# Kernel tuning notes

Hardware: AMD Instinct MI355X
Metric: run time of the kernel (lower is better)

## Reference

```python
import jax, jax.numpy as jnp
import numpy as np

D_MODEL = 512; N_LAYERS = 12; D_STATE = 64; D_CONV = 4; EXPAND = 2
HEADDIM = 64; KLEN = 10
D_INNER = EXPAND * D_MODEL              # 1024
NHEADS = D_INNER // HEADDIM             # 16
CONV_DIM = D_INNER + 2 * D_STATE        # 1152
D_IN_PROJ = 2 * D_INNER + 2 * D_STATE + NHEADS  # 2192
CHUNK = 128; EPS = 1e-5
B_SZ = 2; SEQ = 2048


def rmsnorm(x, w):
    return x * jax.lax.rsqrt(jnp.mean(x * x, axis=-1, keepdims=True) + EPS) * w


def nerf_pe(x):
    # NeRF positional encoding of raw 3D coords, zero-padded to D_MODEL
    nf = D_MODEL // (2 * x.shape[-1])  # 85 freqs per coord -> 510 dims
    freqs = 2.0 ** jnp.arange(nf, dtype=x.dtype)
    ang = x[..., None] * freqs                       # [B,L,3,nf]
    pe = jnp.concatenate([jnp.sin(ang), jnp.cos(ang)], axis=-1)
    pe = pe.reshape(*x.shape[:-1], -1)               # [B,L,510]
    return jnp.pad(pe, ((0, 0), (0, 0), (0, D_MODEL - pe.shape[-1])))


def ssd(xh, dt, A, Bm, Cm):
    # Chunked Mamba2 SSD selective scan.
    # xh [B,L,H,P], dt [B,L,H] (post-softplus), A [H] (negative), Bm/Cm [B,L,N]
    Bb, L, H, P = xh.shape; N = Bm.shape[-1]; C = L // CHUNK
    xh = xh.reshape(Bb, C, CHUNK, H, P)
    dt = dt.reshape(Bb, C, CHUNK, H)
    Bm = Bm.reshape(Bb, C, CHUNK, N)
    Cm = Cm.reshape(Bb, C, CHUNK, N)
    a = dt * A                                   # [B,C,Q,H], <= 0
    a_cum = jnp.cumsum(a, axis=2)
    # intra-chunk decay L[i,j] = exp(a_cum_i - a_cum_j), i >= j
    diff = a_cum[:, :, :, None, :] - a_cum[:, :, None, :, :]  # [B,C,i,j,H]
    tri = jnp.tril(jnp.ones((CHUNK, CHUNK), bool))
    Lmat = jnp.where(tri[None, None, :, :, None], jnp.exp(diff), 0.0)
    scores = jnp.einsum('bcin,bcjn->bcij', Cm, Bm)
    M = scores[..., None] * Lmat * dt[:, :, None, :, :]       # [B,C,i,j,H]
    y_diag = jnp.einsum('bcijh,bcjhp->bcihp', M, xh)
    # per-chunk end states
    a_sum = a_cum[:, :, -1, :]                                # [B,C,H]
    dstate = jnp.exp(a_sum[:, :, None, :] - a_cum) * dt       # [B,C,Q,H]
    S = jnp.einsum('bcjh,bcjn,bcjhp->bchpn', dstate, Bm, xh)  # [B,C,H,P,N]
    dec = jnp.exp(a_sum)

    def step(h, inp):
        Sc, dc = inp
        return h * dc[:, :, None, None] + Sc, h  # emit state BEFORE this chunk

    h0 = jnp.zeros((Bb, H, P, N), xh.dtype)
    _, hs = jax.lax.scan(step, h0, (S.transpose(1, 0, 2, 3, 4), dec.transpose(1, 0, 2)))
    y_off = jnp.einsum('bcih,bcin,cbhpn->bcihp', jnp.exp(a_cum), Cm, hs)
    return (y_diag + y_off).reshape(Bb, L, H, P)


def mamba_block(x, in_w, conv_w, conv_b, dt_b, A_log, Dp, gw, out_w):
    Bb, L, _ = x.shape
    zxbcdt = x @ in_w                             # [B,L,2192]
    z = zxbcdt[..., :D_INNER]
    xBC = zxbcdt[..., D_INNER:D_INNER + CONV_DIM]
    dt = zxbcdt[..., D_INNER + CONV_DIM:]
    # causal depthwise conv1d, kernel D_CONV
    xp = jnp.pad(xBC, ((0, 0), (D_CONV - 1, 0), (0, 0)))
    xc = sum(xp[:, k:k + L, :] * conv_w[:, k] for k in range(D_CONV)) + conv_b
    xc = jax.nn.silu(xc)
    xh = xc[..., :D_INNER].reshape(Bb, L, NHEADS, HEADDIM)
    Bm = xc[..., D_INNER:D_INNER + D_STATE]
    Cm = xc[..., D_INNER + D_STATE:]
    dt = jax.nn.softplus(dt + dt_b)
    A = -jnp.exp(A_log)
    y = ssd(xh, dt, A, Bm, Cm) + Dp[None, None, :, None] * xh
    y = y.reshape(Bb, L, D_INNER)
    y = rmsnorm(y * jax.nn.silu(z), gw)           # gated RMSNorm
    return y @ out_w


def setup_inputs() -> dict:
    key = jax.random.key(0)
    ks = jax.random.split(key, 8)
    s = 0.02
    x = jax.random.normal(ks[0], (B_SZ, SEQ, 3), jnp.float32)
    W_embed = jax.random.normal(ks[1], (3, D_MODEL), jnp.float32) * s
    rms_w = jnp.ones((N_LAYERS, D_MODEL), jnp.float32)
    in_proj_w = jax.random.normal(ks[2], (N_LAYERS, D_MODEL, D_IN_PROJ), jnp.float32) * s
    conv_w = jax.random.normal(ks[3], (N_LAYERS, CONV_DIM, D_CONV), jnp.float32) * s
    conv_b = jnp.zeros((N_LAYERS, CONV_DIM), jnp.float32)
    dt_bias = jax.random.normal(ks[4], (N_LAYERS, NHEADS), jnp.float32) * 0.1
    A_log = jnp.log(jnp.broadcast_to(jnp.arange(1, NHEADS + 1, dtype=jnp.float32), (N_LAYERS, NHEADS)))
    D_param = jnp.ones((N_LAYERS, NHEADS), jnp.float32)
    gnorm_w = jnp.ones((N_LAYERS, D_INNER), jnp.float32)
    out_proj_w = jax.random.normal(ks[5], (N_LAYERS, D_INNER, D_MODEL), jnp.float32) * s
    final_norm_w = jnp.ones((D_MODEL,), jnp.float32)
    head_w = jax.random.normal(ks[6], (D_MODEL, KLEN * 3), jnp.float32) * s
    head_b = jnp.zeros((KLEN * 3,), jnp.float32)
    return dict(x=x, W_embed=W_embed, rms_w=rms_w, in_proj_w=in_proj_w,
                conv_w=conv_w, conv_b=conv_b, dt_bias=dt_bias, A_log=A_log,
                D_param=D_param, gnorm_w=gnorm_w, out_proj_w=out_proj_w,
                final_norm_w=final_norm_w, head_w=head_w, head_b=head_b)


def reference(x, W_embed, rms_w, in_proj_w, conv_w, conv_b, dt_bias, A_log,
              D_param, gnorm_w, out_proj_w, final_norm_w, head_w, head_b):
    x = jnp.where(x == -100.0, 0.0, x)            # change_maskval
    h = x @ W_embed + nerf_pe(x)                  # EmbedderAdd

    def layer(h, p):
        rw, iw, cw, cb, db, al, dp, gw, ow = p
        z = mamba_block(rmsnorm(h, rw), iw, cw, cb, db, al, dp, gw, ow)
        return h + z, None                        # dropout is identity in eval

    h, _ = jax.lax.scan(layer, h, (rms_w, in_proj_w, conv_w, conv_b, dt_bias,
                                   A_log, D_param, gnorm_w, out_proj_w))
    h = rmsnorm(h, final_norm_w)
    return h @ head_w + head_b                    # [B,L,30]
```

## Files before the change

### kernel.cpp

```cpp
#include <hip/hip_runtime.h>
#include <math.h>

#define DM 512
#define DSTATE 64
#define HD 64
#define DI 1024
#define NH 16
#define CONVD 1152
#define DIP 2192
#define CHK 128
#define NCH 16
#define BSZ 2
#define SEQL 2048
#define BL (BSZ*SEQL)
#define NLAYER 12
#define EPSF 1e-5f
#define NPAD_IN 2304

typedef __attribute__((ext_vector_type(4))) float f32x4;
typedef __attribute__((ext_vector_type(8))) short s16x8;

__device__ __forceinline__ float bf2f(ushort u) {
    union { unsigned int i; float f; } v; v.i = ((unsigned int)u) << 16; return v.f;
}
__device__ __forceinline__ ushort f2bf(float f) {
    union { float f; unsigned int u; } v; v.f = f;
    unsigned int u = v.u;
    unsigned int r = (u + 0x7fffu + ((u >> 16) & 1u)) >> 16;
    return (ushort)r;
}

#define GLOAD_LDS16(gptr, lptr) __builtin_amdgcn_global_load_lds( \
    (const __attribute__((address_space(1))) void*)(gptr), \
    (__attribute__((address_space(3))) void*)(lptr), 16, 0, 0)

#define MFMA_BF16(a, b, c) __builtin_amdgcn_mfma_f32_16x16x32_bf16(a, b, c, 0, 0, 0)

__global__ void embed_kernel(const float* __restrict__ x, const float* __restrict__ W,
                             float* __restrict__ h) {
    int tok = blockIdx.x;
    float xe[3];
#pragma unroll
    for (int e = 0; e < 3; e++) {
        float v = x[tok * 3 + e];
        xe[e] = (v == -100.0f) ? 0.0f : v;
    }
    for (int d = threadIdx.x; d < DM; d += blockDim.x) {
        float pe = 0.0f;
        if (d < 510) {
            int e = d / 170, r = d % 170;
            int is_sin = (r < 85);
            int k = is_sin ? r : r - 85;
            float ang = xe[e] * ldexpf(1.0f, k);
            double dv = is_sin ? sin((double)ang) : cos((double)ang);
            pe = (float)dv;
        }
        float acc = pe;
#pragma unroll
        for (int e = 0; e < 3; e++) acc += xe[e] * W[e * DM + d];
        h[(size_t)tok * DM + d] = acc;
    }
}

__global__ __launch_bounds__(256) void rmsnorm512_bf_kernel(const float* __restrict__ in,
                                                            const float* __restrict__ w,
                                                            ushort* __restrict__ out) {
    int tok = blockIdx.x;
    const float* row = in + (size_t)tok * DM;
    float v0 = row[threadIdx.x];
    float v1 = row[threadIdx.x + 256];
    float ss = v0 * v0 + v1 * v1;
    for (int o = 32; o; o >>= 1) ss += __shfl_down(ss, o);
    __shared__ float sbuf[4];
    if ((threadIdx.x & 63) == 0) sbuf[threadIdx.x >> 6] = ss;
    __syncthreads();
    if (threadIdx.x == 0) {
        float s = sbuf[0] + sbuf[1] + sbuf[2] + sbuf[3];
        sbuf[0] = rsqrtf(s / (float)DM + EPSF);
    }
    __syncthreads();
    float rs = sbuf[0];
    ushort* orow = out + (size_t)tok * DM;
    orow[threadIdx.x] = f2bf(v0 * rs * w[threadIdx.x]);
    orow[threadIdx.x + 256] = f2bf(v1 * rs * w[threadIdx.x + 256]);
}

__global__ __launch_bounds__(256) void gatenorm_kernel(const float* __restrict__ y,
                                                       const ushort* __restrict__ zx,
                                                       const float* __restrict__ gw,
                                                       ushort* __restrict__ yb) {
    int tok = blockIdx.x;
    const ushort* zrow = zx + (size_t)tok * DIP;
    const float* yrow = y + (size_t)tok * DI;
    float v[4];
    float ss = 0.0f;
#pragma unroll
    for (int k = 0; k < 4; k++) {
        int d = threadIdx.x + k * 256;
        float z = bf2f(zrow[d]);
        float s = z / (1.0f + __expf(-z));
        float val = yrow[d] * s;
        v[k] = val;
        ss += val * val;
    }
    for (int o = 32; o; o >>= 1) ss += __shfl_down(ss, o);
    __shared__ float sbuf[4];
    if ((threadIdx.x & 63) == 0) sbuf[threadIdx.x >> 6] = ss;
    __syncthreads();
    if (threadIdx.x == 0) {
        float s = sbuf[0] + sbuf[1] + sbuf[2] + sbuf[3];
        sbuf[0] = rsqrtf(s / (float)DI + EPSF);
    }
    __syncthreads();
    float rs = sbuf[0];
    ushort* ob = yb + (size_t)tok * DI;
#pragma unroll
    for (int k = 0; k < 4; k++) {
        int d = threadIdx.x + k * 256;
        ob[d] = f2bf(v[k] * rs * gw[d]);
    }
}

__global__ __launch_bounds__(256) void convT_kernel(const float* __restrict__ w,
                                                    ushort* __restrict__ wT,
                                                    int K, int N, int Npad) {
    __shared__ ushort tile[64][65];
    int l = blockIdx.z;
    int n0 = blockIdx.x * 64, k0 = blockIdx.y * 64;
    const float* src = w + (size_t)l * K * N;
    ushort* dst = wT + (size_t)l * Npad * K;
    int tid = threadIdx.x;
#pragma unroll
    for (int t = 0; t < 16; t++) {
        int idx = tid + t * 256;
        int r = idx >> 6, c = idx & 63;
        float v = (n0 + c < N) ? src[(size_t)(k0 + r) * N + n0 + c] : 0.0f;
        tile[c][r] = f2bf(v);
    }
    __syncthreads();
#pragma unroll
    for (int t = 0; t < 16; t++) {
        int idx = tid + t * 256;
        int r = idx >> 6, c = idx & 63;
        dst[(size_t)(n0 + r) * K + k0 + c] = tile[r][c];
    }
}

template <int MODE, int MT>
__global__ __launch_bounds__(256) void gemm_bf16_kernel(
    const ushort* __restrict__ A, const ushort* __restrict__ BT,
    ushort* __restrict__ Cb, float* __restrict__ Cf, float* __restrict__ aux,
    int N, int Nstride, int K)
{
    __shared__ ushort As[2][MT * 32 * 64];
    __shared__ ushort Bs[2][128 * 64];
    int nwg = gridDim.x * gridDim.y;
    int w0 = blockIdx.y * gridDim.x + blockIdx.x;
    int wg = (w0 & 7) * (nwg >> 3) + (w0 >> 3);
    int by = wg / gridDim.x, bx = wg - by * gridDim.x;
    int bm = by * (MT * 32), bn = bx * 128;
    int tid = threadIdx.x;
    int lane = tid & 63, wid = tid >> 6;
    int wr = wid >> 1, wc = wid & 1;
    int r15 = lane & 15, q = lane >> 4;
    f32x4 acc[MT][4] = {};
    const int nkt = K >> 6;

#define STAGE_GEMM(b, kt) do {                                              \
        int k0s = (kt) << 6;                                                \
        _Pragma("unroll")                                                   \
        for (int t = 0; t < MT; t++) {                                      \
            int cbase = wid * (MT * 64) + t * 64;                           \
            int chunk = cbase + lane;                                       \
            int row = chunk >> 3, s = chunk & 7;                            \
            int kc = s ^ (row & 7);                                         \
            GLOAD_LDS16(A + (size_t)(bm + row) * K + k0s + kc * 8,          \
                        &As[b][cbase * 8]);                                 \
        }                                                                   \
        _Pragma("unroll")                                                   \
        for (int t = 0; t < 4; t++) {                                       \
            int cbase = wid * 256 + t * 64;                                 \
            int chunk = cbase + lane;                                       \
            int row = chunk >> 3, s = chunk & 7;                            \
            int kc = s ^ (row & 7);                                         \
            GLOAD_LDS16(BT + (size_t)(bn + row) * K + k0s + kc * 8,         \
                        &Bs[b][cbase * 8]);                                 \
        }                                                                   \
    } while (0)

    STAGE_GEMM(0, 0);
    __syncthreads();
    for (int kt = 0; kt < nkt; kt++) {
        int cur = kt & 1;
        if (kt + 1 < nkt) STAGE_GEMM(cur ^ 1, kt + 1);
        const ushort* Ac = As[cur];
        const ushort* Bc = Bs[cur];
#pragma unroll
        for (int kh = 0; kh < 2; kh++) {
            s16x8 av[MT], bv[4];
#pragma unroll
            for (int m = 0; m < MT; m++) {
                int row = wr * (MT * 16) + m * 16 + r15;
                int s = (kh * 4 + q) ^ (row & 7);
                av[m] = *(const s16x8*)(Ac + row * 64 + s * 8);
            }
#pragma unroll
            for (int n = 0; n < 4; n++) {
                int row = wc * 64 + n * 16 + r15;
                int s = (kh * 4 + q) ^ (row & 7);
                bv[n] = *(const s16x8*)(Bc + row * 64 + s * 8);
            }
#pragma unroll
            for (int m = 0; m < MT; m++)
#pragma unroll
                for (int n = 0; n < 4; n++)
                    acc[m][n] = MFMA_BF16(av[m], bv[n], acc[m][n]);
        }
        __syncthreads();
    }
#undef STAGE_GEMM

#pragma unroll
    for (int m = 0; m < MT; m++) {
        int row0 = bm + wr * (MT * 16) + m * 16 + q * 4;
#pragma unroll
        for (int n = 0; n < 4; n++) {
            int col = bn + wc * 64 + n * 16 + r15;
#pragma unroll
            for (int r = 0; r < 4; r++) {
                float v = acc[m][n][r];
                int rr = row0 + r;
                if (MODE == 0) {
                    if (col < N) {
                        Cb[(size_t)rr * Nstride + col] = f2bf(v);
                        if (col >= DI + CONVD) aux[(size_t)rr * 16 + (col - DI - CONVD)] = v;
                    }
                } else if (MODE == 1) {
                    Cf[(size_t)rr * Nstride + col] += v;
                } else {
                    if (col < N) Cf[(size_t)rr * Nstride + col] = v + aux[col];
                }
            }
        }
    }
}

__global__ __launch_bounds__(256) void conv_kernel(const ushort* __restrict__ zx,
                                                   const float* __restrict__ cw,
                                                   const float* __restrict__ cb,
                                                   ushort* __restrict__ xc) {
    int gid = blockIdx.x * 256 + threadIdx.x;
    int cu = gid % (CONVD / 8);
    int rb = gid / (CONVD / 8);
    int c8 = cu * 8;
    int l0 = rb * 4;
    int lmod = l0 & (SEQL - 1);

    float wk[4][8];
    const float4* wp = (const float4*)(cw + c8 * 4);
#pragma unroll
    for (int e = 0; e < 8; e++) {
        float4 v = wp[e];
        wk[0][e] = v.x; wk[1][e] = v.y; wk[2][e] = v.z; wk[3][e] = v.w;
    }
    float4 b0 = *(const float4*)(cb + c8);
    float4 b1 = *(const float4*)(cb + c8 + 4);
    float bias[8] = {b0.x, b0.y, b0.z, b0.w, b1.x, b1.y, b1.z, b1.w};

    const ushort* base = zx + (size_t)l0 * DIP + DI + c8;
    s16x8 zero = {};
    s16x8 rows[7];
    rows[0] = (lmod >= 3) ? *(const s16x8*)(base - 3 * DIP) : zero;
    rows[1] = (lmod >= 2) ? *(const s16x8*)(base - 2 * DIP) : zero;
    rows[2] = (lmod >= 1) ? *(const s16x8*)(base - 1 * DIP) : zero;
#pragma unroll
    for (int r = 0; r < 4; r++) rows[3 + r] = *(const s16x8*)(base + (size_t)r * DIP);

    ushort* ob = xc + (size_t)l0 * CONVD + c8;
#pragma unroll
    for (int r = 0; r < 4; r++) {
        s16x8 o;
#pragma unroll
        for (int e = 0; e < 8; e++) {
            float a = bias[e];
#pragma unroll
            for (int k = 0; k < 4; k++)
                a += bf2f((ushort)rows[r + k][e]) * wk[k][e];
            float s = a / (1.0f + __expf(-a));
            o[e] = (short)f2bf(s);
        }
        *(s16x8*)(ob + (size_t)r * CONVD) = o;
    }
}

__global__ __launch_bounds__(512, 4) void ssd1_kernel(
    const ushort* __restrict__ xc, const float* __restrict__ dtraw,
    const float* __restrict__ dt_bias, const float* __restrict__ A_log,
    const float* __restrict__ Dp, float* __restrict__ acg,
    float* __restrict__ decbuf, float* __restrict__ y, float* __restrict__ S)
{
    __shared__ ushort Mb[128 * 128];
    __shared__ ushort xhT[64 * 136];
    __shared__ ushort BmT[64 * 136];
    __shared__ float sAc[128], sDt[128], sDs[128];
    __shared__ float s_wsum, s_stot;

    int hh = blockIdx.x, bc = blockIdx.y;
    int tid = threadIdx.x, lane = tid & 63, w = tid >> 6;
    int l15 = lane & 15, lq = lane >> 4;
    int bch = bc * NH + hh;
    const size_t xbase = (size_t)(bc * CHK) * CONVD;
    ushort* Cs = Mb;
    ushort* Bs = Mb + 8192;
    float Dh = Dp[hh];

#pragma unroll
    for (int t = 0; t < 2; t++) {
        int cbase = t * 512 + w * 64;
        int chunk = cbase + lane;
        int row = chunk >> 3, s = chunk & 7;
        int kc = s ^ (row & 7);
        GLOAD_LDS16(xc + xbase + (size_t)row * CONVD + DI + DSTATE + kc * 8, Cs + (size_t)cbase * 8);
        GLOAD_LDS16(xc + xbase + (size_t)row * CONVD + DI + kc * 8, Bs + (size_t)cbase * 8);
    }
    {
        int j = tid & 127, pc = tid >> 7;
#pragma unroll
        for (int it = 0; it < 2; it++) {
            int pc8 = pc * 2 + it;
            s16x8 vx = *(const s16x8*)(xc + xbase + (size_t)j * CONVD + hh * HD + pc8 * 8);
            s16x8 vb = *(const s16x8*)(xc + xbase + (size_t)j * CONVD + DI + pc8 * 8);
#pragma unroll
            for (int e = 0; e < 8; e++) {
                int R = pc8 * 8 + e;
                int off = R * 136 + (((j >> 3) ^ (R & 7)) << 3) + (j & 7);
                xhT[off] = (ushort)vx[e];
                BmT[off] = (ushort)vb[e];
            }
        }
    }
    float v_scan = 0.0f, dt_v = 0.0f;
    if (tid < 128) {
        float raw = dtraw[(size_t)(bc * CHK + tid) * 16 + hh] + dt_bias[hh];
        dt_v = raw > 0.0f ? raw + log1pf(__expf(-raw)) : log1pf(__expf(raw));
        v_scan = dt_v * (-__expf(A_log[hh]));
#pragma unroll
        for (int o = 1; o < 64; o <<= 1) {
            float u = __shfl_up(v_scan, o);
            if (lane >= o) v_scan += u;
        }
        if (tid == 63) s_wsum = v_scan;
    }
    __syncthreads();

    float ac_v = 0.0f;
    if (tid < 128) {
        ac_v = (tid >= 64) ? v_scan + s_wsum : v_scan;
        if (tid == 127) s_stot = ac_v;
    }
    f32x4 acc_s[8] = {};
    {
        int row = w * 16 + l15;
#pragma unroll
        for (int kh = 0; kh < 2; kh++) {
            int sl = (kh * 4 + lq) ^ (row & 7);
            s16x8 av = *(const s16x8*)(Cs + row * 64 + sl * 8);
#pragma unroll
            for (int nj = 0; nj < 8; nj++) {
                int jr = nj * 16 + l15;
                int sl2 = (kh * 4 + lq) ^ (jr & 7);
                s16x8 bv = *(const s16x8*)(Bs + jr * 64 + sl2 * 8);
                acc_s[nj] = MFMA_BF16(av, bv, acc_s[nj]);
            }
        }
    }
    __syncthreads();

    if (tid < 128) {
        float asum = s_stot;
        sAc[tid] = ac_v;
        sDt[tid] = dt_v;
        sDs[tid] = __expf(asum - ac_v) * dt_v;
        acg[(size_t)bch * CHK + tid] = ac_v;
        if (tid == 0) decbuf[bch] = __expf(asum);
    }
    __syncthreads();

#pragma unroll
    for (int nj = 0; nj < 8; nj++) {
        int j = nj * 16 + l15;
        if (nj < w) {
            float acj = sAc[j], dtj = sDt[j];
#pragma unroll
            for (int r = 0; r < 4; r++) {
                int i = w * 16 + lq * 4 + r;
                float v = acc_s[nj][r] * __expf(sAc[i] - acj) * dtj;
                Mb[i * 128 + ((((i & 7) ^ (j >> 3)) << 3) | (j & 7))] = f2bf(v);
            }
        } else if (nj == w) {
            float acj = sAc[j], dtj = sDt[j];
#pragma unroll
            for (int r = 0; r < 4; r++) {
                int i = w * 16 + lq * 4 + r;
                float v;
                if (j < i)       v = acc_s[nj][r] * __expf(sAc[i] - acj) * dtj;
                else if (j == i) v = acc_s[nj][r] * dtj + Dh;
                else             v = 0.0f;
                Mb[i * 128 + ((((i & 7) ^ (j >> 3)) << 3) | (j & 7))] = f2bf(v);
            }
        } else if (nj == w + 1) {
#pragma unroll
            for (int r = 0; r < 4; r++) {
                int i = w * 16 + lq * 4 + r;
                Mb[i * 128 + ((((i & 7) ^ (j >> 3)) << 3) | (j & 7))] = 0;
            }
        }
    }
    {
        int j = tid & 127, g = tid >> 7;
        float dsj = sDs[j];
#pragma unroll
        for (int rr = 0; rr < 16; rr++) {
            int R = g * 16 + rr;
            int off = R * 136 + (((j >> 3) ^ (R & 7)) << 3) + (j & 7);
            BmT[off] = f2bf(bf2f(BmT[off]) * dsj);
        }
    }
    __syncthreads();

    int ph = w >> 2, iq = w & 3;
    f32x4 acc_y[2][2] = {};
    f32x4 acc_st[2] = {};
    int nn = iq * 16 + l15;
#pragma unroll
    for (int ks = 0; ks < 4; ks++) {
        int cj = ks * 4 + lq;
        s16x8 axh[2];
#pragma unroll
        for (int m = 0; m < 2; m++) {
            int p = ph * 32 + m * 16 + l15;
            axh[m] = *(const s16x8*)(xhT + p * 136 + ((cj ^ (p & 7)) << 3));
        }
        s16x8 bb = *(const s16x8*)(BmT + nn * 136 + ((cj ^ (nn & 7)) << 3));
#pragma unroll
        for (int m = 0; m < 2; m++)
            acc_st[m] = MFMA_BF16(axh[m], bb, acc_st[m]);
        if (ks <= iq) {
            s16x8 bm_[2];
#pragma unroll
            for (int n = 0; n < 2; n++) {
                int i = iq * 32 + n * 16 + l15;
                bm_[n] = *(const s16x8*)(Mb + i * 128 + ((cj ^ (i & 7)) << 3));
            }
#pragma unroll
            for (int m = 0; m < 2; m++)
#pragma unroll
                for (int n = 0; n < 2; n++)
                    acc_y[m][n] = MFMA_BF16(axh[m], bm_[n], acc_y[m][n]);
        }
    }

#pragma unroll
    for (int m = 0; m < 2; m++) {
        int p0 = ph * 32 + m * 16 + lq * 4;
#pragma unroll
        for (int n = 0; n < 2; n++) {
            int i = iq * 32 + n * 16 + l15;
            *(f32x4*)&y[(size_t)(bc * CHK + i) * DI + hh * HD + p0] = acc_y[m][n];
        }
#pragma unroll
        for (int r = 0; r < 4; r++)
            S[(size_t)bch * 4096 + (size_t)(p0 + r) * 64 + nn] = acc_st[m][r];
    }
}

__global__ __launch_bounds__(256) void ssd2_kernel(
    const ushort* __restrict__ xc, const float* __restrict__ Sg,
    const float* __restrict__ decg, const float* __restrict__ acg,
    float* __restrict__ y)
{
    __shared__ ushort Cs[128 * 64];
    __shared__ ushort Hs[64 * 64];
    __shared__ float sAc[128];
    int hh = blockIdx.x, bc = blockIdx.y;
    int tid = threadIdx.x, lane = tid & 63, wid = tid >> 6;
    int wr = wid >> 1, wc = wid & 1, l15 = lane & 15, lq = lane >> 4;
    int bch = bc * NH + hh;
    int b = bc >> 4, cc = bc & 15;
    const size_t xbase = (size_t)(bc * CHK) * CONVD;
#pragma unroll
    for (int t = 0; t < 4; t++) {
        int cbase = t * 256 + wid * 64;
        int chunk = cbase + lane;
        int row = chunk >> 3, s = chunk & 7;
        int kc = s ^ (row & 7);
        GLOAD_LDS16(xc + xbase + (size_t)row * CONVD + DI + DSTATE + kc * 8, Cs + (size_t)cbase * 8);
    }
    {
        int p = tid >> 2, n0 = (tid & 3) * 16;
        f32x4 acc4[4] = {};
        float wgt = 1.0f;
        for (int c = cc - 1; c >= 0; --c) {
            int bch_c = (b * NCH + c) * NH + hh;
            const float* src = Sg + (size_t)bch_c * 4096 + p * 64 + n0;
            float dv = decg[bch_c];
#pragma unroll
            for (int q2 = 0; q2 < 4; q2++) {
                f32x4 sv = *(const f32x4*)(src + q2 * 4);
                acc4[q2].x += sv.x * wgt; acc4[q2].y += sv.y * wgt;
                acc4[q2].z += sv.z * wgt; acc4[q2].w += sv.w * wgt;
            }
            wgt *= dv;
        }
#pragma unroll
        for (int g = 0; g < 2; g++) {
            int nch = (n0 >> 3) + g;
            int s = nch ^ (p & 7);
            ushort* dst = Hs + p * 64 + s * 8;
#pragma unroll
            for (int ee = 0; ee < 8; ee++) {
                int idx = g * 8 + ee;
                dst[ee] = f2bf(acc4[idx >> 2][idx & 3]);
            }
        }
    }
    if (tid < 128) sAc[tid] = acg[(size_t)bch * CHK + tid];
    __syncthreads();
    f32x4 acc[2][4] = {};
#pragma unroll
    for (int kh = 0; kh < 2; kh++) {
        s16x8 av[2], bv[4];
#pragma unroll
        for (int m = 0; m < 2; m++) {
            int p = wr * 32 + m * 16 + l15;
            int sl = (kh * 4 + lq) ^ (p & 7);
            av[m] = *(const s16x8*)(Hs + p * 64 + sl * 8);
        }
#pragma unroll
        for (int n = 0; n < 4; n++) {
            int i = wc * 64 + n * 16 + l15;
            int sl = (kh * 4 + lq) ^ (i & 7);
            bv[n] = *(const s16x8*)(Cs + i * 64 + sl * 8);
        }
#pragma unroll
        for (int m = 0; m < 2; m++)
#pragma unroll
            for (int n = 0; n < 4; n++)
                acc[m][n] = MFMA_BF16(av[m], bv[n], acc[m][n]);
    }
#pragma unroll
    for (int m = 0; m < 2; m++) {
        int p0 = wr * 32 + m * 16 + lq * 4;
#pragma unroll
        for (int n = 0; n < 4; n++) {
            int i = wc * 64 + n * 16 + l15;
            float e = __expf(sAc[i]);
            float* dst = &y[(size_t)(bc * CHK + i) * DI + hh * HD + p0];
            f32x4 v = *(f32x4*)dst;
#pragma unroll
            for (int r = 0; r < 4; r++) v[r] += e * acc[m][n][r];
            *(f32x4*)dst = v;
        }
    }
}

extern "C" void kernel_launch(void* const* d_in, const int* in_sizes, int n_in,
                              void* d_out, int out_size, void* d_ws, size_t ws_size,
                              hipStream_t stream) {
    const float* x        = (const float*)d_in[0];
    const float* W_embed  = (const float*)d_in[1];
    const float* rms_w    = (const float*)d_in[2];
    const float* in_w     = (const float*)d_in[3];
    const float* conv_w   = (const float*)d_in[4];
    const float* conv_b   = (const float*)d_in[5];
    const float* dt_bias  = (const float*)d_in[6];
    const float* A_log    = (const float*)d_in[7];
    const float* D_param  = (const float*)d_in[8];
    const float* gnorm_w  = (const float*)d_in[9];
    const float* out_w    = (const float*)d_in[10];
    const float* fnorm_w  = (const float*)d_in[11];
    const float* head_w   = (const float*)d_in[12];
    const float* head_b   = (const float*)d_in[13];
    float* out = (float*)d_out;

    char* p = (char*)d_ws;
    auto alloc = [&](size_t bytes) { char* r = p; p += (bytes + 255) & ~(size_t)255; return r; };

    float*  h_buf   = (float*)alloc((size_t)BL * DM * 4);
    float*  y_buf   = (float*)alloc((size_t)BL * DI * 4);
    float*  S_buf   = (float*)alloc((size_t)BSZ * NCH * NH * HD * DSTATE * 4);
    float*  ac_buf  = (float*)alloc((size_t)BSZ * NCH * NH * CHK * 4);
    float*  dec_buf = (float*)alloc((size_t)BSZ * NCH * NH * 4);
    float*  dtraw   = (float*)alloc((size_t)BL * 16 * 4);
    ushort* xn_bf   = (ushort*)alloc((size_t)BL * DM * 2);
    ushort* zx_bf   = (ushort*)alloc((size_t)BL * DIP * 2);
    ushort* xc_bf   = (ushort*)alloc((size_t)BL * CONVD * 2);
    ushort* y_bf    = (ushort*)alloc((size_t)BL * DI * 2);
    ushort* headT   = (ushort*)alloc((size_t)128 * DM * 2);

    size_t in_full  = (size_t)NLAYER * NPAD_IN * DM * 2;
    size_t out_full = (size_t)NLAYER * DM * DI * 2;
    size_t used = (size_t)(p - (char*)d_ws);
    bool full = (used + in_full + out_full + 4096) <= ws_size;
    ushort* inT  = (ushort*)alloc(full ? in_full  : (size_t)NPAD_IN * DM * 2);
    ushort* outT = (ushort*)alloc(full ? out_full : (size_t)DM * DI * 2);

    embed_kernel<<<BL, 256, 0, stream>>>(x, W_embed, h_buf);
    convT_kernel<<<dim3(2, DM / 64, 1), 256, 0, stream>>>(head_w, headT, DM, 30, 128);
    if (full) {
        convT_kernel<<<dim3(NPAD_IN / 64, DM / 64, NLAYER), 256, 0, stream>>>(
            in_w, inT, DM, DIP, NPAD_IN);
        convT_kernel<<<dim3(DM / 64, DI / 64, NLAYER), 256, 0, stream>>>(
            out_w, outT, DI, DM, DM);
    }

    for (int l = 0; l < NLAYER; l++) {
        const float* rw = rms_w + (size_t)l * DM;
        const float* cw = conv_w + (size_t)l * CONVD * 4;
        const float* cb = conv_b + (size_t)l * CONVD;
        const float* db = dt_bias + (size_t)l * NH;
        const float* al = A_log + (size_t)l * NH;
        const float* dp = D_param + (size_t)l * NH;
        const float* gw = gnorm_w + (size_t)l * DI;

        ushort* inT_l  = full ? inT  + (size_t)l * NPAD_IN * DM : inT;
        ushort* outT_l = full ? outT + (size_t)l * DM * DI      : outT;
        if (!full) {
            convT_kernel<<<dim3(NPAD_IN / 64, DM / 64, 1), 256, 0, stream>>>(
                in_w + (size_t)l * DM * DIP, inT_l, DM, DIP, NPAD_IN);
            convT_kernel<<<dim3(DM / 64, DI / 64, 1), 256, 0, stream>>>(
                out_w + (size_t)l * DI * DM, outT_l, DI, DM, DM);
        }

        rmsnorm512_bf_kernel<<<BL, 256, 0, stream>>>(h_buf, rw, xn_bf);
        gemm_bf16_kernel<0, 2><<<dim3(NPAD_IN / 128, BL / 64), 256, 0, stream>>>(
            xn_bf, inT_l, zx_bf, nullptr, dtraw, DIP, DIP, DM);
        conv_kernel<<<((BL / 4) * (CONVD / 8)) / 256, 256, 0, stream>>>(zx_bf, cw, cb, xc_bf);
        ssd1_kernel<<<dim3(NH, BSZ * NCH), 512, 0, stream>>>(xc_bf, dtraw, db, al, dp,
                                                             ac_buf, dec_buf, y_buf, S_buf);
        ssd2_kernel<<<dim3(NH, BSZ * NCH), 256, 0, stream>>>(xc_bf, S_buf, dec_buf,
                                                             ac_buf, y_buf);
        gatenorm_kernel<<<BL, 256, 0, stream>>>(y_buf, zx_bf, gw, y_bf);
        gemm_bf16_kernel<1, 1><<<dim3(DM / 128, BL / 32), 256, 0, stream>>>(
            y_bf, outT_l, nullptr, h_buf, nullptr, DM, DM, DI);
    }

    rmsnorm512_bf_kernel<<<BL, 256, 0, stream>>>(h_buf, fnorm_w, xn_bf);
    gemm_bf16_kernel<2, 4><<<dim3(1, BL / 128), 256, 0, stream>>>(
        xn_bf, headT, nullptr, out, (float*)head_b, 30, 30, DM);
}
```

Baseline: 1.249 ms.

## Vectorize row norms to one wave per row and shrink GEMM tiles

The RMSNorm and gated-norm kernels now give each 64-lane wave a whole row. They use vector loads and stores and reduce with a wave-wide xor shuffle, which removes the shared-memory step and both block barriers. The bf16 GEMM gains an N-tile template parameter. The in-projection, out-projection and head GEMMs now use smaller M or N tiles, so more workgroups are launched and the head GEMM does less padded-column work. Smaller tiles lower operand reuse per workgroup and may add global traffic in exchange for better occupancy.

```diff
diff --git a/kernel.cpp b/kernel.cpp
--- a/kernel.cpp
+++ b/kernel.cpp
@@ -65,60 +65,60 @@
 __global__ __launch_bounds__(256) void rmsnorm512_bf_kernel(const float* __restrict__ in,
                                                             const float* __restrict__ w,
                                                             ushort* __restrict__ out) {
-    int tok = blockIdx.x;
-    const float* row = in + (size_t)tok * DM;
-    float v0 = row[threadIdx.x];
-    float v1 = row[threadIdx.x + 256];
-    float ss = v0 * v0 + v1 * v1;
-    for (int o = 32; o; o >>= 1) ss += __shfl_down(ss, o);
-    __shared__ float sbuf[4];
-    if ((threadIdx.x & 63) == 0) sbuf[threadIdx.x >> 6] = ss;
-    __syncthreads();
-    if (threadIdx.x == 0) {
-        float s = sbuf[0] + sbuf[1] + sbuf[2] + sbuf[3];
-        sbuf[0] = rsqrtf(s / (float)DM + EPSF);
-    }
-    __syncthreads();
-    float rs = sbuf[0];
-    ushort* orow = out + (size_t)tok * DM;
-    orow[threadIdx.x] = f2bf(v0 * rs * w[threadIdx.x]);
-    orow[threadIdx.x + 256] = f2bf(v1 * rs * w[threadIdx.x + 256]);
+    int row = blockIdx.x * 4 + (threadIdx.x >> 6);
+    int lane = threadIdx.x & 63;
+    const float* r = in + (size_t)row * DM + lane * 8;
+    f32x4 a = *(const f32x4*)r;
+    f32x4 b = *(const f32x4*)(r + 4);
+    float ss = a.x*a.x + a.y*a.y + a.z*a.z + a.w*a.w
+             + b.x*b.x + b.y*b.y + b.z*b.z + b.w*b.w;
+#pragma unroll
+    for (int o = 32; o; o >>= 1) ss += __shfl_xor(ss, o);
+    float rs = rsqrtf(ss / (float)DM + EPSF);
+    const float* wp = w + lane * 8;
+    f32x4 w0 = *(const f32x4*)wp;
+    f32x4 w1 = *(const f32x4*)(wp + 4);
+    s16x8 o8;
+    o8[0] = (short)f2bf(a.x * rs * w0.x); o8[1] = (short)f2bf(a.y * rs * w0.y);
+    o8[2] = (short)f2bf(a.z * rs * w0.z); o8[3] = (short)f2bf(a.w * rs * w0.w);
+    o8[4] = (short)f2bf(b.x * rs * w1.x); o8[5] = (short)f2bf(b.y * rs * w1.y);
+    o8[6] = (short)f2bf(b.z * rs * w1.z); o8[7] = (short)f2bf(b.w * rs * w1.w);
+    *(s16x8*)(out + (size_t)row * DM + lane * 8) = o8;
 }
 
 __global__ __launch_bounds__(256) void gatenorm_kernel(const float* __restrict__ y,
                                                        const ushort* __restrict__ zx,
                                                        const float* __restrict__ gw,
                                                        ushort* __restrict__ yb) {
-    int tok = blockIdx.x;
-    const ushort* zrow = zx + (size_t)tok * DIP;
-    const float* yrow = y + (size_t)tok * DI;
-    float v[4];
+    int row = blockIdx.x * 4 + (threadIdx.x >> 6);
+    int lane = threadIdx.x & 63;
+    const float* yp = y + (size_t)row * DI + lane * 16;
+    const ushort* zp = zx + (size_t)row * DIP + lane * 16;
+    s16x8 z0 = *(const s16x8*)zp;
+    s16x8 z1 = *(const s16x8*)(zp + 8);
+    float v[16];
     float ss = 0.0f;
 #pragma unroll
-    for (int k = 0; k < 4; k++) {
-        int d = threadIdx.x + k * 256;
-        float z = bf2f(zrow[d]);
+    for (int e = 0; e < 16; e++) {
+        float z = bf2f((ushort)(e < 8 ? z0[e] : z1[e - 8]));
         float s = z / (1.0f + __expf(-z));
-        float val = yrow[d] * s;
-        v[k] = val;
+        float val = yp[e] * s;
+        v[e] = val;
         ss += val * val;
     }
-    for (int o = 32; o; o >>= 1) ss += __shfl_down(ss, o);
-    __shared__ float sbuf[4];
-    if ((threadIdx.x & 63) == 0) sbuf[threadIdx.x >> 6] = ss;
-    __syncthreads();
-    if (threadIdx.x == 0) {
-        float s = sbuf[0] + sbuf[1] + sbuf[2] + sbuf[3];
-        sbuf[0] = rsqrtf(s / (float)DI + EPSF);
-    }
-    __syncthreads();
-    float rs = sbuf[0];
-    ushort* ob = yb + (size_t)tok * DI;
-#pragma unroll
-    for (int k = 0; k < 4; k++) {
-        int d = threadIdx.x + k * 256;
-        ob[d] = f2bf(v[k] * rs * gw[d]);
-    }
+#pragma unroll
+    for (int o = 32; o; o >>= 1) ss += __shfl_xor(ss, o);
+    float rs = rsqrtf(ss / (float)DI + EPSF);
+    const float* gp = gw + lane * 16;
+    s16x8 oa, ob;
+#pragma unroll
+    for (int e = 0; e < 8; e++) {
+        oa[e] = (short)f2bf(v[e] * rs * gp[e]);
+        ob[e] = (short)f2bf(v[e + 8] * rs * gp[e + 8]);
+    }
+    ushort* op = yb + (size_t)row * DI + lane * 16;
+    *(s16x8*)op = oa;
+    *(s16x8*)(op + 8) = ob;
 }
 
 __global__ __launch_bounds__(256) void convT_kernel(const float* __restrict__ w,
@@ -146,24 +146,24 @@
     }
 }
 
-template <int MODE, int MT>
+template <int MODE, int MT, int NT>
 __global__ __launch_bounds__(256) void gemm_bf16_kernel(
     const ushort* __restrict__ A, const ushort* __restrict__ BT,
     ushort* __restrict__ Cb, float* __restrict__ Cf, float* __restrict__ aux,
     int N, int Nstride, int K)
 {
     __shared__ ushort As[2][MT * 32 * 64];
-    __shared__ ushort Bs[2][128 * 64];
+    __shared__ ushort Bs[2][NT * 32 * 64];
     int nwg = gridDim.x * gridDim.y;
     int w0 = blockIdx.y * gridDim.x + blockIdx.x;
     int wg = (w0 & 7) * (nwg >> 3) + (w0 >> 3);
     int by = wg / gridDim.x, bx = wg - by * gridDim.x;
-    int bm = by * (MT * 32), bn = bx * 128;
+    int bm = by * (MT * 32), bn = bx * (NT * 32);
     int tid = threadIdx.x;
     int lane = tid & 63, wid = tid >> 6;
     int wr = wid >> 1, wc = wid & 1;
     int r15 = lane & 15, q = lane >> 4;
-    f32x4 acc[MT][4] = {};
+    f32x4 acc[MT][NT] = {};
     const int nkt = K >> 6;
 
 #define STAGE_GEMM(b, kt) do {                                              \
@@ -178,8 +178,8 @@
                         &As[b][cbase * 8]);                                 \
         }                                                                   \
         _Pragma("unroll")                                                   \
-        for (int t = 0; t < 4; t++) {                                       \
-            int cbase = wid * 256 + t * 64;                                 \
+        for (int t = 0; t < NT; t++) {                                      \
+            int cbase = wid * (NT * 64) + t * 64;                           \
             int chunk = cbase + lane;                                       \
             int row = chunk >> 3, s = chunk & 7;                            \
             int kc = s ^ (row & 7);                                         \
@@ -197,7 +197,7 @@
         const ushort* Bc = Bs[cur];
 #pragma unroll
         for (int kh = 0; kh < 2; kh++) {
-            s16x8 av[MT], bv[4];
+            s16x8 av[MT], bv[NT];
 #pragma unroll
             for (int m = 0; m < MT; m++) {
                 int row = wr * (MT * 16) + m * 16 + r15;
@@ -205,15 +205,15 @@
                 av[m] = *(const s16x8*)(Ac + row * 64 + s * 8);
             }
 #pragma unroll
-            for (int n = 0; n < 4; n++) {
-                int row = wc * 64 + n * 16 + r15;
+            for (int n = 0; n < NT; n++) {
+                int row = wc * (NT * 16) + n * 16 + r15;
                 int s = (kh * 4 + q) ^ (row & 7);
                 bv[n] = *(const s16x8*)(Bc + row * 64 + s * 8);
             }
 #pragma unroll
             for (int m = 0; m < MT; m++)
 #pragma unroll
-                for (int n = 0; n < 4; n++)
+                for (int n = 0; n < NT; n++)
                     acc[m][n] = MFMA_BF16(av[m], bv[n], acc[m][n]);
         }
         __syncthreads();
@@ -224,8 +224,8 @@
     for (int m = 0; m < MT; m++) {
         int row0 = bm + wr * (MT * 16) + m * 16 + q * 4;
 #pragma unroll
-        for (int n = 0; n < 4; n++) {
-            int col = bn + wc * 64 + n * 16 + r15;
+        for (int n = 0; n < NT; n++) {
+            int col = bn + wc * (NT * 16) + n * 16 + r15;
 #pragma unroll
             for (int r = 0; r < 4; r++) {
                 float v = acc[m][n][r];
@@ -632,20 +632,20 @@
                 out_w + (size_t)l * DI * DM, outT_l, DI, DM, DM);
         }
 
-        rmsnorm512_bf_kernel<<<BL, 256, 0, stream>>>(h_buf, rw, xn_bf);
-        gemm_bf16_kernel<0, 2><<<dim3(NPAD_IN / 128, BL / 64), 256, 0, stream>>>(
+        rmsnorm512_bf_kernel<<<BL / 4, 256, 0, stream>>>(h_buf, rw, xn_bf);
+        gemm_bf16_kernel<0, 1, 4><<<dim3(NPAD_IN / 128, BL / 32), 256, 0, stream>>>(
             xn_bf, inT_l, zx_bf, nullptr, dtraw, DIP, DIP, DM);
         conv_kernel<<<((BL / 4) * (CONVD / 8)) / 256, 256, 0, stream>>>(zx_bf, cw, cb, xc_bf);
         ssd1_kernel<<<dim3(NH, BSZ * NCH), 512, 0, stream>>>(xc_bf, dtraw, db, al, dp,
                                                              ac_buf, dec_buf, y_buf, S_buf);
         ssd2_kernel<<<dim3(NH, BSZ * NCH), 256, 0, stream>>>(xc_bf, S_buf, dec_buf,
                                                              ac_buf, y_buf);
-        gatenorm_kernel<<<BL, 256, 0, stream>>>(y_buf, zx_bf, gw, y_bf);
-        gemm_bf16_kernel<1, 1><<<dim3(DM / 128, BL / 32), 256, 0, stream>>>(
+        gatenorm_kernel<<<BL / 4, 256, 0, stream>>>(y_buf, zx_bf, gw, y_bf);
+        gemm_bf16_kernel<1, 1, 2><<<dim3(DM / 64, BL / 32), 256, 0, stream>>>(
             y_bf, outT_l, nullptr, h_buf, nullptr, DM, DM, DI);
     }
 
-    rmsnorm512_bf_kernel<<<BL, 256, 0, stream>>>(h_buf, fnorm_w, xn_bf);
-    gemm_bf16_kernel<2, 4><<<dim3(1, BL / 128), 256, 0, stream>>>(
+    rmsnorm512_bf_kernel<<<BL / 4, 256, 0, stream>>>(h_buf, fnorm_w, xn_bf);
+    gemm_bf16_kernel<2, 4, 1><<<dim3(1, BL / 128), 256, 0, stream>>>(
         xn_bf, headT, nullptr, out, (float*)head_b, 30, 30, DM);
 }
```

New measurement: 1.222 ms. -2.2%, faster.
